# Kernel tuning notes

Measured on AMD Instinct MI355X. Metric: run time of the kernel, lower is better.

Reference implementation:

```python
import jax, jax.numpy as jnp
import numpy as np

EPS = 1.0  # Shapelet eps
STRIDE = 1


def _shapelet(x, w, pcm):
    """x: (b,c,t), w: (n,c,l), pcm: (c,m). Returns ((b, n*c) probs, (b, n*c) dists)."""
    n, c, l = w.shape
    t = x.shape[-1]
    m = (t - l) // STRIDE + 1
    # unfold: gather overlapping windows -> (b, c, m, l)
    idx = jnp.arange(m)[:, None] * STRIDE + jnp.arange(l)[None, :]
    win = x[:, :, idx]                                   # (b, c, m, l)
    xw = jnp.transpose(win, (0, 2, 1, 3))[:, :, None]    # (b, m, 1, c, l)
    d = jnp.mean(jnp.abs(xw - w), axis=-1)               # (b, m, n, c)
    d = d * pcm.T[None, :, None, :]                      # penalty (1, m, 1, c)
    p = jnp.exp(-jnp.square(EPS * d))                    # (b, m, n, c)
    hard = jax.nn.one_hot(jnp.argmax(p, axis=1), m, axis=1, dtype=p.dtype)  # (b,m,n,c)
    soft = jax.nn.softmax(p, axis=1)
    onehot_max = hard + soft - jax.lax.stop_gradient(soft)  # straight-through
    max_p = jnp.sum(onehot_max * p, axis=1)              # (b, n, c)
    d_min = jnp.min(d, axis=1)                           # (b, n, c)
    b = x.shape[0]
    return max_p.reshape(b, -1), d_min.reshape(b, -1)


def _diversity(w):
    """w: (n,c,l) -> scalar. torch PairwiseDistance(p=2, eps=1e-6) adds eps to diff."""
    sh = jnp.transpose(w, (1, 0, 2))                     # (c, n, l)
    diff = sh[:, None, :, :] - sh[:, :, None, :] + 1e-6
    dist = jnp.sqrt(jnp.sum(jnp.square(diff), axis=-1))  # (c, n, n)
    nsh = sh.shape[1]
    mask = 1.0 - jnp.eye(nsh, dtype=w.dtype)
    return jnp.mean(jnp.exp(-dist) * mask[None])


def setup_inputs() -> dict:
    key = jax.random.key(0)
    ks = jax.random.split(key, 6)
    b, c, t, ncls = 32, 8, 512, 10
    sls = [52, 103, 154, 256]
    ms = [t - l + 1 for l in sls]
    inp = {"x": jax.random.normal(ks[0], (b, c, t), dtype=jnp.float32)}
    for i, (l, m) in enumerate(zip(sls, ms)):
        inp[f"w{i}"] = jax.random.normal(ks[1 + i], (5, c, l), dtype=jnp.float32)
        inp[f"pcm{i}"] = jnp.ones((c, m), dtype=jnp.float32)
    inp["W_out"] = jax.random.normal(ks[5], (ncls, 160), dtype=jnp.float32) * 0.05
    return inp


def reference(x, w0, w1, w2, w3, pcm0, pcm1, pcm2, pcm3, W_out):
    # instance norm over time (torch std is unbiased, ddof=1)
    mu = jnp.mean(x, axis=-1, keepdims=True)
    sd = jnp.std(x, axis=-1, keepdims=True, ddof=1)
    xn = (x - mu) / (sd + 1e-8)

    ws = (w0, w1, w2, w3)
    pcms = (pcm0, pcm1, pcm2, pcm3)
    probs, dists = [], []
    for w, pcm in zip(ws, pcms):
        p, d = _shapelet(xn, w, pcm)
        probs.append(p)
        dists.append(d)
    shapelet_probs = jnp.concatenate(probs, axis=-1)   # (b, 160)
    shapelet_dists = jnp.concatenate(dists, axis=-1)   # (b, 160)

    # dropout is identity in eval mode
    out = shapelet_probs @ W_out.T                     # (b, num_classes)

    loss_reg = jnp.mean(jnp.abs(W_out))
    loss_div = sum(_diversity(w) for w in ws)
    loss = (0.1 * loss_reg + 0.1 * loss_div).reshape(1)
    return out, shapelet_dists, shapelet_probs, loss
```

## Files before the change

kernel.cpp:

```cpp
#include <hip/hip_runtime.h>
#include <math.h>

#define B 32
#define C 8
#define T 512
#define NSH 5
#define NCLS 10
#define NFEAT 160

#define OUT_OFF    0
#define DIST_OFF   (B * NCLS)
#define PROB_OFF   (DIST_OFF + B * NFEAT)
#define LOSS_OFF   (PROB_OFF + B * NFEAT)

#define XN_OFF   1024
#define XSTRIDE  520
#define P3_OFF   200000
#define P2_OFF   212800
#define P1_OFF   228160
#define P0_OFF   246080

__global__ __launch_bounds__(256) void prep_kernel(
    const float* __restrict__ x,
    const float* __restrict__ w0, const float* __restrict__ w1,
    const float* __restrict__ w2, const float* __restrict__ w3,
    const float* __restrict__ Wout,
    float* __restrict__ wsf)
{
    const int blk  = blockIdx.x;
    const int tid  = threadIdx.x;
    const int wv   = __builtin_amdgcn_readfirstlane(tid >> 6);
    const int lane = tid & 63;

    if (blk < 64) {
        const int bc = blk * 4 + wv;
        const float* xr = x + bc * T;
        const float4 u0 = *(const float4*)(xr + lane * 4);
        const float4 u1 = *(const float4*)(xr + 256 + lane * 4);
        float s = u0.x + u0.y + u0.z + u0.w + u1.x + u1.y + u1.z + u1.w;
        #pragma unroll
        for (int off = 32; off; off >>= 1) s += __shfl_down(s, off);
        const float mu = __shfl(s, 0) * (1.0f / T);
        float sq = (u0.x-mu)*(u0.x-mu) + (u0.y-mu)*(u0.y-mu) + (u0.z-mu)*(u0.z-mu) + (u0.w-mu)*(u0.w-mu)
                 + (u1.x-mu)*(u1.x-mu) + (u1.y-mu)*(u1.y-mu) + (u1.z-mu)*(u1.z-mu) + (u1.w-mu)*(u1.w-mu);
        #pragma unroll
        for (int off = 32; off; off >>= 1) sq += __shfl_down(sq, off);
        const float var = __shfl(sq, 0) * (1.0f / (T - 1));
        const float ns  = 1.0f / (sqrtf(var) + 1e-8f);
        const float nbv = -mu * ns;
        float* xo = wsf + XN_OFF + bc * XSTRIDE;
        const float4 o0 = { fmaf(u0.x,ns,nbv), fmaf(u0.y,ns,nbv), fmaf(u0.z,ns,nbv), fmaf(u0.w,ns,nbv) };
        const float4 o1 = { fmaf(u1.x,ns,nbv), fmaf(u1.y,ns,nbv), fmaf(u1.z,ns,nbv), fmaf(u1.w,ns,nbv) };
        *(float4*)(xo + lane * 4)       = o0;
        *(float4*)(xo + 256 + lane * 4) = o1;
        if (lane < 2) *(float4*)(xo + T + lane * 4) = float4{0.f, 0.f, 0.f, 0.f};
    } else if (blk < 224) {
        const int task = (blk - 64) * 4 + wv;
        const int g  = task / 160;
        const int r  = task - g * 160;
        const int c  = r / 20;
        const int pr = r - c * 20;
        const int i  = pr >> 2;
        const int j0 = pr & 3;
        const int j  = j0 + (j0 >= i ? 1 : 0);
        const float* wptrs[4] = { w0, w1, w2, w3 };
        const int    Ls[4]    = { 52, 103, 154, 256 };
        const int L = Ls[g];
        const float* wi = wptrs[g] + (i * C + c) * L;
        const float* wj = wptrs[g] + (j * C + c) * L;
        float ss = 0.0f;
        for (int t2 = lane; t2 < L; t2 += 64) {
            const float df = wj[t2] - wi[t2] + 1e-6f;
            ss += df * df;
        }
        #pragma unroll
        for (int off = 32; off; off >>= 1) ss += __shfl_down(ss, off);
        if (lane == 0) wsf[task] = expf(-sqrtf(ss));
    } else {
        float rg = 0.0f;
        #pragma unroll
        for (int k2 = 0; k2 < 7; ++k2) {
            const int e = lane + k2 * 64;
            if (e < 400) rg += fabsf(Wout[wv * 400 + e]);
        }
        #pragma unroll
        for (int off = 32; off; off >>= 1) rg += __shfl_down(rg, off);
        if (lane == 0) wsf[640 + wv] = rg;
    }
}

template<int L, int M, int S>
__device__ __forceinline__ void shapelet_task(
    const float* __restrict__ xn,
    const float* __restrict__ wg,
    const float* __restrict__ pmg,
    float* __restrict__ part,
    int r)
{
    constexpr int CL = C * L;
    const int lane = threadIdx.x & 63;
    const int bc = r / S;
    const int ms = r - bc * S;
    const int c  = bc & 7;
    const int m  = ms * 64 + lane;
    const bool act = (m < M);
    const int mm = act ? m : 0;
    const float* xr = xn + bc * XSTRIDE + mm;
    const float* wr = wg + c * L;

    float acc[5] = {0, 0, 0, 0, 0};

    constexpr int NB  = L / 8;
    constexpr int REM = L % 8;

    float xfA[8], xfB[8];
    float cwA[5][8], cwB[5][8];

    #pragma unroll
    for (int q = 0; q < 8; ++q) xfA[q] = xr[q];
    #pragma unroll
    for (int n = 0; n < 5; ++n) {
        #pragma unroll
        for (int q = 0; q < 8; ++q) cwA[n][q] = wr[n * CL + q];
    }

#define STEP(CUR_X, CUR_W, NXT_X, NXT_W, IT)                                \
    {                                                                       \
        const int jn = ((IT) + 1 < NB) ? ((IT) + 1) * 8 : 0;                \
        _Pragma("unroll")                                                   \
        for (int q = 0; q < 8; ++q) NXT_X[q] = xr[(IT) * 8 + 8 + q];        \
        _Pragma("unroll")                                                   \
        for (int n = 0; n < 5; ++n) {                                       \
            _Pragma("unroll")                                               \
            for (int q = 0; q < 8; ++q) NXT_W[n][q] = wr[n * CL + jn + q];  \
        }                                                                   \
        _Pragma("unroll")                                                   \
        for (int jj = 0; jj < 8; ++jj) {                                    \
            const float xv = CUR_X[jj];                                     \
            _Pragma("unroll")                                               \
            for (int n = 0; n < 5; ++n)                                     \
                acc[n] += fabsf(xv - CUR_W[n][jj]);                         \
        }                                                                   \
    }

    int it = 0;
    for (; it + 2 <= NB; it += 2) {
        STEP(xfA, cwA, xfB, cwB, it)
        STEP(xfB, cwB, xfA, cwA, it + 1)
    }
    if constexpr ((NB & 1) != 0) {
        STEP(xfA, cwA, xfB, cwB, NB - 1)
    }
#undef STEP

    if constexpr (REM > 0) {
        float xt[8];
        float wt5[5][8];
        #pragma unroll
        for (int q = 0; q < REM; ++q) xt[q] = xr[NB * 8 + q];
        #pragma unroll
        for (int n = 0; n < 5; ++n) {
            #pragma unroll
            for (int q = 0; q < REM; ++q) wt5[n][q] = wr[n * CL + NB * 8 + q];
        }
        #pragma unroll
        for (int jj = 0; jj < REM; ++jj) {
            const float xv = xt[jj];
            #pragma unroll
            for (int n = 0; n < 5; ++n) acc[n] += fabsf(xv - wt5[n][jj]);
        }
    }

    const float pmv = pmg[c * M + mm];
    constexpr float invL = 1.0f / (float)L;
    const float scale = invL * pmv;

    float dv[5], d2[5];
    #pragma unroll
    for (int n = 0; n < 5; ++n) {
        dv[n] = act ? acc[n] * scale : INFINITY;
        d2[n] = act ? dv[n] * dv[n] : INFINITY;
    }

    #pragma unroll
    for (int off = 32; off; off >>= 1) {
        #pragma unroll
        for (int n = 0; n < 5; ++n) {
            dv[n] = fminf(dv[n], __shfl_down(dv[n], off));
            d2[n] = fminf(d2[n], __shfl_down(d2[n], off));
        }
    }
    if (lane == 0) {
        #pragma unroll
        for (int n = 0; n < 5; ++n) {
            float* p = part + ((bc * 5 + n) * S + ms) * 2;
            p[0] = dv[n];
            p[1] = d2[n];
        }
    }
}

__global__ __launch_bounds__(256) void shapelet_kernel(
    const float* __restrict__ xn,
    const float* __restrict__ w0, const float* __restrict__ w1,
    const float* __restrict__ w2, const float* __restrict__ w3,
    const float* __restrict__ p0, const float* __restrict__ p1,
    const float* __restrict__ p2, const float* __restrict__ p3,
    float* __restrict__ part0, float* __restrict__ part1,
    float* __restrict__ part2, float* __restrict__ part3)
{
    const int wv = __builtin_amdgcn_readfirstlane(threadIdx.x >> 6);
    const int wt = blockIdx.x * 4 + wv;

    if (wt < 1280)
        shapelet_task<256, 257, 5>(xn, w3, p3, part3, wt);
    else if (wt < 2816)
        shapelet_task<154, 359, 6>(xn, w2, p2, part2, wt - 1280);
    else if (wt < 4608)
        shapelet_task<103, 410, 7>(xn, w1, p1, part1, wt - 2816);
    else
        shapelet_task< 52, 461, 8>(xn, w0, p0, part0, wt - 4608);
}

__global__ __launch_bounds__(256) void head2_kernel(
    const float* __restrict__ Wout,
    const float* __restrict__ wsf,
    float* __restrict__ out)
{
    const int blk = blockIdx.x;
    const int tid = threadIdx.x;

    if (blk < B) {
        const int b = blk;
        __shared__ float pl[NFEAT];
        if (tid < NFEAT) {
            const int col = tid;
            const int g   = col / 40;
            const int rem = col - g * 40;
            const int n   = rem >> 3;
            const int c   = rem & 7;
            const int bc  = b * C + c;
            int S, pbase;
            switch (g) {
                case 0:  S = 8; pbase = P0_OFF; break;
                case 1:  S = 7; pbase = P1_OFF; break;
                case 2:  S = 6; pbase = P2_OFF; break;
                default: S = 5; pbase = P3_OFF; break;
            }
            const float* p = wsf + pbase + ((bc * 5 + n) * S) * 2;
            float mnd = INFINITY, mn2 = INFINITY;
            for (int msi = 0; msi < S; ++msi) {
                mnd = fminf(mnd, p[msi * 2]);
                mn2 = fminf(mn2, p[msi * 2 + 1]);
            }
            out[DIST_OFF + b * NFEAT + col] = mnd;
            const float pb = expf(-mn2);
            out[PROB_OFF + b * NFEAT + col] = pb;
            pl[col] = pb;
        }
        __syncthreads();
        if (tid < NFEAT) {
            const int k = tid >> 4, seg = tid & 15;
            const float* wr = Wout + k * NFEAT + seg * 10;
            const float* pp = pl + seg * 10;
            float acc = 0.0f;
            #pragma unroll
            for (int q = 0; q < 10; ++q) acc += pp[q] * wr[q];
            #pragma unroll
            for (int off = 8; off; off >>= 1) acc += __shfl_down(acc, off, 16);
            if (seg == 0) out[OUT_OFF + b * NCLS + k] = acc;
        }
    } else if (tid < 64) {
        const int lane = tid;
        float dv = 0.0f, rg = 0.0f;
        #pragma unroll
        for (int r = 0; r < 10; ++r) dv += wsf[lane + r * 64];
        if (lane < 4) rg = wsf[640 + lane];
        #pragma unroll
        for (int off = 32; off; off >>= 1) {
            dv += __shfl_down(dv, off);
            rg += __shfl_down(rg, off);
        }
        if (lane == 0)
            out[LOSS_OFF] = 0.1f * (rg * (1.0f / 1600.0f)) + 0.1f * (dv * (1.0f / 200.0f));
    }
}

extern "C" void kernel_launch(void* const* d_in, const int* in_sizes, int n_in,
                              void* d_out, int out_size, void* d_ws, size_t ws_size,
                              hipStream_t stream) {
    const float* x    = (const float*)d_in[0];
    const float* w0   = (const float*)d_in[1];
    const float* pcm0 = (const float*)d_in[2];
    const float* w1   = (const float*)d_in[3];
    const float* pcm1 = (const float*)d_in[4];
    const float* w2   = (const float*)d_in[5];
    const float* pcm2 = (const float*)d_in[6];
    const float* w3   = (const float*)d_in[7];
    const float* pcm3 = (const float*)d_in[8];
    const float* Wout = (const float*)d_in[9];
    float* out = (float*)d_out;
    float* wsf = (float*)d_ws;

    prep_kernel<<<225, 256, 0, stream>>>(x, w0, w1, w2, w3, Wout, wsf);
    shapelet_kernel<<<1664, 256, 0, stream>>>(
        wsf + XN_OFF, w0, w1, w2, w3, pcm0, pcm1, pcm2, pcm3,
        wsf + P0_OFF, wsf + P1_OFF, wsf + P2_OFF, wsf + P3_OFF);
    head2_kernel<<<B + 1, 256, 0, stream>>>(Wout, wsf, out);
}
```

Measured before the change: 99.68 us.

## Share sliding-window x values across lanes with ds_bpermute instead of global loads

Each wave now loads its strip of the normalized series into registers once, NR values per lane. In the fully unrolled inner loop it reconstructs each shifted window element with two ds_bpermute cross-lane shuffles and a select. This replaces the old per-lane overlapping global loads and their double-buffered prefetch, moving x traffic from the vector memory/L1 path to the LDS crossbar. Costs are two bpermutes per window element, a very large unrolled body for L=256, and reads that run slightly past the row end into padding or the next row.

After: 118.3 us. +18.6%, slower.

```diff
diff --git a/kernel.cpp b/kernel.cpp
--- a/kernel.cpp
+++ b/kernel.cpp
@@ -89,7 +89,7 @@
     }
 }
 
-template<int L, int M, int S>
+template<int L, int M, int S, int NR>
 __device__ __forceinline__ void shapelet_task(
     const float* __restrict__ xn,
     const float* __restrict__ wg,
@@ -105,70 +105,33 @@
     const int m  = ms * 64 + lane;
     const bool act = (m < M);
     const int mm = act ? m : 0;
-    const float* xr = xn + bc * XSTRIDE + mm;
+    const float* xrow = xn + bc * XSTRIDE + ms * 64;
     const float* wr = wg + c * L;
 
+    int xreg[NR];
+    #pragma unroll
+    for (int k = 0; k < NR; ++k)
+        xreg[k] = __float_as_int(xrow[64 * k + lane]);
+
+    const int lane4 = lane * 4;
     float acc[5] = {0, 0, 0, 0, 0};
 
-    constexpr int NB  = L / 8;
-    constexpr int REM = L % 8;
-
-    float xfA[8], xfB[8];
-    float cwA[5][8], cwB[5][8];
-
-    #pragma unroll
-    for (int q = 0; q < 8; ++q) xfA[q] = xr[q];
-    #pragma unroll
-    for (int n = 0; n < 5; ++n) {
-        #pragma unroll
-        for (int q = 0; q < 8; ++q) cwA[n][q] = wr[n * CL + q];
-    }
-
-#define STEP(CUR_X, CUR_W, NXT_X, NXT_W, IT)                                \
-    {                                                                       \
-        const int jn = ((IT) + 1 < NB) ? ((IT) + 1) * 8 : 0;                \
-        _Pragma("unroll")                                                   \
-        for (int q = 0; q < 8; ++q) NXT_X[q] = xr[(IT) * 8 + 8 + q];        \
-        _Pragma("unroll")                                                   \
-        for (int n = 0; n < 5; ++n) {                                       \
-            _Pragma("unroll")                                               \
-            for (int q = 0; q < 8; ++q) NXT_W[n][q] = wr[n * CL + jn + q];  \
-        }                                                                   \
-        _Pragma("unroll")                                                   \
-        for (int jj = 0; jj < 8; ++jj) {                                    \
-            const float xv = CUR_X[jj];                                     \
-            _Pragma("unroll")                                               \
-            for (int n = 0; n < 5; ++n)                                     \
-                acc[n] += fabsf(xv - CUR_W[n][jj]);                         \
-        }                                                                   \
-    }
-
-    int it = 0;
-    for (; it + 2 <= NB; it += 2) {
-        STEP(xfA, cwA, xfB, cwB, it)
-        STEP(xfB, cwB, xfA, cwA, it + 1)
-    }
-    if constexpr ((NB & 1) != 0) {
-        STEP(xfA, cwA, xfB, cwB, NB - 1)
-    }
-#undef STEP
-
-    if constexpr (REM > 0) {
-        float xt[8];
-        float wt5[5][8];
-        #pragma unroll
-        for (int q = 0; q < REM; ++q) xt[q] = xr[NB * 8 + q];
-        #pragma unroll
-        for (int n = 0; n < 5; ++n) {
-            #pragma unroll
-            for (int q = 0; q < REM; ++q) wt5[n][q] = wr[n * CL + NB * 8 + q];
-        }
-        #pragma unroll
-        for (int jj = 0; jj < REM; ++jj) {
-            const float xv = xt[jj];
-            #pragma unroll
-            for (int n = 0; n < 5; ++n) acc[n] += fabsf(xv - wt5[n][jj]);
-        }
+    #pragma unroll
+    for (int J = 0; J < L; ++J) {
+        const int k0  = J >> 6;
+        const int rem = J & 63;
+        float xv;
+        if (rem == 0) {
+            xv = __int_as_float(xreg[k0]);
+        } else {
+            const int addr = lane4 + J * 4;
+            const int va = __builtin_amdgcn_ds_bpermute(addr, xreg[k0]);
+            const int vb = __builtin_amdgcn_ds_bpermute(addr, xreg[k0 + 1]);
+            xv = __int_as_float((lane < 64 - rem) ? va : vb);
+        }
+        #pragma unroll
+        for (int n = 0; n < 5; ++n)
+            acc[n] += fabsf(xv - wr[n * CL + J]);
     }
 
     const float pmv = pmg[c * M + mm];
@@ -213,13 +176,13 @@
     const int wt = blockIdx.x * 4 + wv;
 
     if (wt < 1280)
-        shapelet_task<256, 257, 5>(xn, w3, p3, part3, wt);
+        shapelet_task<256, 257, 5, 5>(xn, w3, p3, part3, wt);
     else if (wt < 2816)
-        shapelet_task<154, 359, 6>(xn, w2, p2, part2, wt - 1280);
+        shapelet_task<154, 359, 6, 4>(xn, w2, p2, part2, wt - 1280);
     else if (wt < 4608)
-        shapelet_task<103, 410, 7>(xn, w1, p1, part1, wt - 2816);
+        shapelet_task<103, 410, 7, 3>(xn, w1, p1, part1, wt - 2816);
     else
-        shapelet_task< 52, 461, 8>(xn, w0, p0, part0, wt - 4608);
+        shapelet_task< 52, 461, 8, 2>(xn, w0, p0, part0, wt - 4608);
 }
 
 __global__ __launch_bounds__(256) void head2_kernel(
```
